# Kernel optimization log

Measured on AMD Instinct MI355X. Metric: run time of the kernel, lower is better.

## Reference

```python
import jax, jax.numpy as jnp
import numpy as np

B, T, I, U, O, BB = 256, 1024, 64, 256, 64, 128  # batch, seq, input, units, output, backbone_units

def lecun_tanh(x):
    return 1.7159 * jnp.tanh(0.666 * x)

def setup_inputs() -> dict:
    key = jax.random.key(0)
    ks = jax.random.split(key, 13)
    def lin(k, fan_in, fan_out):
        bound = 1.0 / np.sqrt(fan_in)
        kw, kb = jax.random.split(k)
        W = jax.random.uniform(kw, (fan_in, fan_out), jnp.float32, -bound, bound)
        b = jax.random.uniform(kb, (fan_out,), jnp.float32, -bound, bound)
        return W, b
    x = jax.random.normal(ks[0], (B, T, I), jnp.float32)
    W_bb, b_bb = lin(ks[1], I + U, BB)   # backbone Linear
    W_ff1, b_ff1 = lin(ks[2], BB, U)
    W_ff2, b_ff2 = lin(ks[3], BB, U)
    W_ta, b_ta = lin(ks[4], BB, U)       # time_a
    W_tb, b_tb = lin(ks[5], BB, U)       # time_b
    W_fc, b_fc = lin(ks[6], U, O)        # readout
    return {"x": x, "W_bb": W_bb, "b_bb": b_bb, "W_ff1": W_ff1, "b_ff1": b_ff1,
            "W_ff2": W_ff2, "b_ff2": b_ff2, "W_ta": W_ta, "b_ta": b_ta,
            "W_tb": W_tb, "b_tb": b_tb, "W_fc": W_fc, "b_fc": b_fc}

def reference(x, W_bb, b_bb, W_ff1, b_ff1, W_ff2, b_ff2, W_ta, b_ta, W_tb, b_tb, W_fc, b_fc):
    ts = jnp.float32(1.0)  # default elapsed time per step
    def step(h, xt):
        z = jnp.concatenate([xt, h], axis=-1)          # [B, I+U]
        g = lecun_tanh(z @ W_bb + b_bb)                # [B, BB]
        ff1 = jnp.tanh(g @ W_ff1 + b_ff1)              # [B, U]
        ff2 = jnp.tanh(g @ W_ff2 + b_ff2)
        t_interp = jax.nn.sigmoid((g @ W_ta + b_ta) * ts + (g @ W_tb + b_tb))
        h_new = ff1 * (1.0 - t_interp) + t_interp * ff2
        return h_new, h_new
    h0 = jnp.zeros((x.shape[0], U), x.dtype)
    h_last, hs = jax.lax.scan(step, h0, jnp.swapaxes(x, 0, 1))  # hs: [T, B, U]
    hs = jnp.swapaxes(hs, 0, 1)                                  # [B, T, U]
    out = hs @ W_fc + b_fc                                       # [B, T, O]
    return out, h_last
```

## Files before the change

kernel.cpp:

```cpp
#include <hip/hip_runtime.h>
#include <stdint.h>

#define B_ 256
#define T_ 1024
#define I_ 64
#define U_ 256
#define O_ 64
#define BB_ 128

typedef unsigned int u32;
typedef unsigned short u16;
typedef _Float16 half2_t __attribute__((ext_vector_type(2)));

#if defined(__has_builtin)
#if __has_builtin(__builtin_amdgcn_fdot2)
#define USE_DOT2 1
#else
#define USE_DOT2 0
#endif
#else
#define USE_DOT2 0
#endif

static __device__ __forceinline__ u32 packpair(float a, float b) {
  half2_t h; h.x = (_Float16)a; h.y = (_Float16)b;
  return __builtin_bit_cast(u32, h);
}
static __device__ __forceinline__ float unpack_lo(u32 u) {
  half2_t h = __builtin_bit_cast(half2_t, u); return (float)h.x;
}
static __device__ __forceinline__ float unpack_hi(u32 u) {
  half2_t h = __builtin_bit_cast(half2_t, u); return (float)h.y;
}
static __device__ __forceinline__ float dot2acc(u32 w, u32 z, float acc) {
#if USE_DOT2
  return __builtin_amdgcn_fdot2(__builtin_bit_cast(half2_t, w),
                                __builtin_bit_cast(half2_t, z), acc, false);
#else
  half2_t hw = __builtin_bit_cast(half2_t, w);
  half2_t hz = __builtin_bit_cast(half2_t, z);
  acc += (float)hw.x * (float)hz.x;
  acc += (float)hw.y * (float)hz.y;
  return acc;
#endif
}

template <int CTRL>
static __device__ __forceinline__ float dpp_mov_f(float v) {
  return __builtin_bit_cast(float, __builtin_amdgcn_update_dpp(
      0, __builtin_bit_cast(int, v), CTRL, 0xF, 0xF, true));
}
#define DPP_XOR1 0xB1
#define DPP_XOR2 0x4E
#define DPP_HMIR 0x141
#define DPP_MIRR 0x140

static __device__ __forceinline__ float fast_tanh(float x) {
  return 1.0f - 2.0f / (1.0f + __expf(2.0f * x));
}
static __device__ __forceinline__ float fast_sigmoid(float x) {
  return 1.0f / (1.0f + __expf(-x));
}

template <bool DEFER>
__global__ __launch_bounds__(1024)
void cfc_kernel(const float* __restrict__ x,
                const float* __restrict__ W_bb, const float* __restrict__ b_bb,
                const float* __restrict__ W_ff1, const float* __restrict__ b_ff1,
                const float* __restrict__ W_ff2, const float* __restrict__ b_ff2,
                const float* __restrict__ W_ta,  const float* __restrict__ b_ta,
                const float* __restrict__ W_tb,  const float* __restrict__ b_tb,
                const float* __restrict__ W_fc,  const float* __restrict__ b_fc,
                float* __restrict__ out, u32* __restrict__ Hbuf)
{
  __shared__ __align__(16) u32 s_z2[160];
  __shared__ __align__(16) u32 s_g2[64];
  u16* s_gh = (u16*)s_g2;

  const int tid = threadIdx.x;
  const int r   = blockIdx.x;

  const int ca  = tid >> 3;
  const int kga = tid & 7;
  const int jb = tid >> 2;
  const int kq = tid & 3;
  const int ro = tid >> 4;
  const int rk = tid & 15;

  u32 wbb[20];
#pragma unroll
  for (int j = 0; j < 5; ++j)
#pragma unroll
    for (int q = 0; q < 4; ++q) {
      int p = 4 * (kga + 8 * j) + q;
      wbb[4 * j + q] = packpair(W_bb[(2 * p) * BB_ + ca],
                                W_bb[(2 * p + 1) * BB_ + ca]);
    }
  u32 wf1[16], wf2[16], wta[16], wtb[16];
#pragma unroll
  for (int j = 0; j < 4; ++j)
#pragma unroll
    for (int q = 0; q < 4; ++q) {
      int p = 4 * (kq + 4 * j) + q;
      int k0 = 2 * p, k1 = 2 * p + 1;
      wf1[4 * j + q] = packpair(W_ff1[k0 * U_ + jb], W_ff1[k1 * U_ + jb]);
      wf2[4 * j + q] = packpair(W_ff2[k0 * U_ + jb], W_ff2[k1 * U_ + jb]);
      wta[4 * j + q] = packpair(W_ta [k0 * U_ + jb], W_ta [k1 * U_ + jb]);
      wtb[4 * j + q] = packpair(W_tb [k0 * U_ + jb], W_tb [k1 * U_ + jb]);
    }
  u32 wfc[8];
  float bfo = 0.f;
  if (!DEFER) {
#pragma unroll
    for (int j = 0; j < 2; ++j)
#pragma unroll
      for (int q = 0; q < 4; ++q) {
        int p = 4 * (rk + 16 * j) + q;
        wfc[4 * j + q] = packpair(W_fc[(2 * p) * O_ + ro],
                                  W_fc[(2 * p + 1) * O_ + ro]);
      }
    bfo = b_fc[ro];
  }
  const float bbbc = b_bb[ca];
  const float b1 = b_ff1[jb], b2 = b_ff2[jb];
  const float bta = b_ta[jb], btb = b_tb[jb];

  const float* xrow = x + (size_t)r * T_ * I_;
  const size_t out_row = (size_t)r * T_ * O_;
  u32* __restrict__ hrow = DEFER ? (Hbuf + (size_t)r * T_ * (U_ / 2)) : nullptr;

  if (tid < 160) s_z2[tid] = 0u;
  __syncthreads();
  if (tid < 32) {
    float2 xv = ((const float2*)xrow)[tid];
    s_z2[tid] = packpair(xv.x, xv.y);
  }
  __syncthreads();

  for (int t = 0; t < T_; ++t) {
    float2 xv;
    const bool ldx = (tid < 32) && (t + 1 < T_);
    if (ldx) xv = ((const float2*)(xrow + (size_t)(t + 1) * I_))[tid];

    float bacc = 0.f;
#pragma unroll
    for (int j = 0; j < 5; ++j) {
      uint4 zz = *reinterpret_cast<const uint4*>(s_z2 + 4 * (kga + 8 * j));
      bacc = dot2acc(wbb[4 * j + 0], zz.x, bacc);
      bacc = dot2acc(wbb[4 * j + 1], zz.y, bacc);
      bacc = dot2acc(wbb[4 * j + 2], zz.z, bacc);
      bacc = dot2acc(wbb[4 * j + 3], zz.w, bacc);
    }
    bacc += dpp_mov_f<DPP_XOR1>(bacc);
    bacc += dpp_mov_f<DPP_XOR2>(bacc);
    bacc += dpp_mov_f<DPP_HMIR>(bacc);
    float g = 1.7159f * fast_tanh(0.666f * (bacc + bbbc));

    float racc = 0.f;
    if (!DEFER) {
#pragma unroll
      for (int j = 0; j < 2; ++j) {
        uint4 hh = *reinterpret_cast<const uint4*>(s_z2 + 32 + 4 * (rk + 16 * j));
        racc = dot2acc(wfc[4 * j + 0], hh.x, racc);
        racc = dot2acc(wfc[4 * j + 1], hh.y, racc);
        racc = dot2acc(wfc[4 * j + 2], hh.z, racc);
        racc = dot2acc(wfc[4 * j + 3], hh.w, racc);
      }
      racc += dpp_mov_f<DPP_XOR1>(racc);
      racc += dpp_mov_f<DPP_XOR2>(racc);
      racc += dpp_mov_f<DPP_HMIR>(racc);
      racc += dpp_mov_f<DPP_MIRR>(racc);
    }
    if ((tid & 7) == 0)
      s_gh[ca] = __builtin_bit_cast(u16, (_Float16)g);
    if (!DEFER && t > 0 && rk == 0)
      out[out_row + (size_t)(t - 1) * O_ + ro] = racc + bfo;
    __syncthreads();

    float a1 = 0.f, a2 = 0.f, a3 = 0.f, a4 = 0.f;
#pragma unroll
    for (int j = 0; j < 4; ++j) {
      uint4 gg = *reinterpret_cast<const uint4*>(s_g2 + 4 * (kq + 4 * j));
      a1 = dot2acc(wf1[4 * j + 0], gg.x, a1);
      a1 = dot2acc(wf1[4 * j + 1], gg.y, a1);
      a1 = dot2acc(wf1[4 * j + 2], gg.z, a1);
      a1 = dot2acc(wf1[4 * j + 3], gg.w, a1);
      a2 = dot2acc(wf2[4 * j + 0], gg.x, a2);
      a2 = dot2acc(wf2[4 * j + 1], gg.y, a2);
      a2 = dot2acc(wf2[4 * j + 2], gg.z, a2);
      a2 = dot2acc(wf2[4 * j + 3], gg.w, a2);
      a3 = dot2acc(wta[4 * j + 0], gg.x, a3);
      a3 = dot2acc(wta[4 * j + 1], gg.y, a3);
      a3 = dot2acc(wta[4 * j + 2], gg.z, a3);
      a3 = dot2acc(wta[4 * j + 3], gg.w, a3);
      a4 = dot2acc(wtb[4 * j + 0], gg.x, a4);
      a4 = dot2acc(wtb[4 * j + 1], gg.y, a4);
      a4 = dot2acc(wtb[4 * j + 2], gg.z, a4);
      a4 = dot2acc(wtb[4 * j + 3], gg.w, a4);
    }
    a1 += dpp_mov_f<DPP_XOR1>(a1); a1 += dpp_mov_f<DPP_XOR2>(a1);
    a2 += dpp_mov_f<DPP_XOR1>(a2); a2 += dpp_mov_f<DPP_XOR2>(a2);
    a3 += dpp_mov_f<DPP_XOR1>(a3); a3 += dpp_mov_f<DPP_XOR2>(a3);
    a4 += dpp_mov_f<DPP_XOR1>(a4); a4 += dpp_mov_f<DPP_XOR2>(a4);
    float f1 = fast_tanh(a1 + b1);
    float f2 = fast_tanh(a2 + b2);
    float ti = fast_sigmoid(a3 + bta + a4 + btb);
    float h  = f1 + ti * (f2 - f1);
    float hq = dpp_mov_f<DPP_HMIR>(h);

    if ((tid & 7) == 0) {
      u32 pr = packpair(h, hq);
      int m = tid >> 3;
      s_z2[32 + m] = pr;
      if (DEFER) hrow[(size_t)t * (U_ / 2) + m] = pr;
    }
    if (ldx) s_z2[tid] = packpair(xv.x, xv.y);
    __syncthreads();
  }

  if (!DEFER) {
    float racc = 0.f;
#pragma unroll
    for (int j = 0; j < 2; ++j) {
      uint4 hh = *reinterpret_cast<const uint4*>(s_z2 + 32 + 4 * (rk + 16 * j));
      racc = dot2acc(wfc[4 * j + 0], hh.x, racc);
      racc = dot2acc(wfc[4 * j + 1], hh.y, racc);
      racc = dot2acc(wfc[4 * j + 2], hh.z, racc);
      racc = dot2acc(wfc[4 * j + 3], hh.w, racc);
    }
    racc += dpp_mov_f<DPP_XOR1>(racc);
    racc += dpp_mov_f<DPP_XOR2>(racc);
    racc += dpp_mov_f<DPP_HMIR>(racc);
    racc += dpp_mov_f<DPP_MIRR>(racc);
    if (rk == 0)
      out[out_row + (size_t)(T_ - 1) * O_ + ro] = racc + bfo;
  }

  if (tid < 128) {
    u32 hp = s_z2[32 + tid];
    float2 hv; hv.x = unpack_lo(hp); hv.y = unpack_hi(hp);
    ((float2*)(out + (size_t)B_ * T_ * O_))[r * 128 + tid] = hv;
  }
}

__global__ __launch_bounds__(512)
void ro_kernel(const u32* __restrict__ Hbuf,
               const float* __restrict__ W_fc, const float* __restrict__ b_fc,
               float* __restrict__ out)
{
  __shared__ __align__(16) u32 s_h[8 * 128];
  const int tid = threadIdx.x;
  const int o   = tid & 63;
  const int w   = tid >> 6;
  const int r   = blockIdx.x;

  u32 wfc[128];
#pragma unroll
  for (int p = 0; p < 128; ++p)
    wfc[p] = packpair(W_fc[(2 * p) * O_ + o], W_fc[(2 * p + 1) * O_ + o]);
  const float bo = b_fc[o];

  const u32* hrow = Hbuf + (size_t)r * T_ * 128;
  const size_t out_row = (size_t)r * T_ * O_;

  for (int c = 0; c < T_ / 8; ++c) {
    *(uint2*)(s_h + 2 * tid) =
        *(const uint2*)(hrow + (size_t)c * 1024 + 2 * tid);
    __syncthreads();
    float acc = bo;
    const uint4* h4 = reinterpret_cast<const uint4*>(s_h + w * 128);
#pragma unroll
    for (int i = 0; i < 32; ++i) {
      uint4 hh = h4[i];
      acc = dot2acc(wfc[4 * i + 0], hh.x, acc);
      acc = dot2acc(wfc[4 * i + 1], hh.y, acc);
      acc = dot2acc(wfc[4 * i + 2], hh.z, acc);
      acc = dot2acc(wfc[4 * i + 3], hh.w, acc);
    }
    out[out_row + (size_t)(8 * c + w) * O_ + o] = acc;
    __syncthreads();
  }
}

extern "C" void kernel_launch(void* const* d_in, const int* in_sizes, int n_in,
                              void* d_out, int out_size, void* d_ws, size_t ws_size,
                              hipStream_t stream) {
  const float* x     = (const float*)d_in[0];
  const float* W_bb  = (const float*)d_in[1];
  const float* b_bb  = (const float*)d_in[2];
  const float* W_ff1 = (const float*)d_in[3];
  const float* b_ff1 = (const float*)d_in[4];
  const float* W_ff2 = (const float*)d_in[5];
  const float* b_ff2 = (const float*)d_in[6];
  const float* W_ta  = (const float*)d_in[7];
  const float* b_ta  = (const float*)d_in[8];
  const float* W_tb  = (const float*)d_in[9];
  const float* b_tb  = (const float*)d_in[10];
  const float* W_fc  = (const float*)d_in[11];
  const float* b_fc  = (const float*)d_in[12];
  float* out = (float*)d_out;

  const size_t h_bytes = (size_t)B_ * T_ * (U_ / 2) * sizeof(u32);
  if (ws_size >= h_bytes) {
    u32* Hbuf = (u32*)d_ws;
    cfc_kernel<true><<<dim3(B_), dim3(1024), 0, stream>>>(
        x, W_bb, b_bb, W_ff1, b_ff1, W_ff2, b_ff2,
        W_ta, b_ta, W_tb, b_tb, W_fc, b_fc, out, Hbuf);
    ro_kernel<<<dim3(B_), dim3(512), 0, stream>>>(Hbuf, W_fc, b_fc, out);
  } else {
    cfc_kernel<false><<<dim3(B_), dim3(1024), 0, stream>>>(
        x, W_bb, b_bb, W_ff1, b_ff1, W_ff2, b_ff2,
        W_ta, b_ta, W_tb, b_tb, W_fc, b_fc, out, nullptr);
  }
}
```

Measured before the change: 1.901 ms.

## Replace per-row recurrent kernel with MFMA kernel processing 16 batch rows per block

Adds a new recurrence kernel in which each 512-thread block handles 16 batch rows and computes the backbone and the three head matmuls with 16x16x32 f16 MFMA instructions. Weights stay in registers as packed f16, and the ta and tb weights are pre-summed so one matmul serves both. The activations use exp2 and reciprocal intrinsics with scale factors folded into the constants. The change trades the previous one-row-per-block scalar and dot2 path, launched as 256 blocks, for matrix cores over only 16 blocks, so it runs on far fewer compute units.

```diff
diff --git a/kernel.cpp b/kernel.cpp
--- a/kernel.cpp
+++ b/kernel.cpp
@@ -11,6 +11,8 @@
 typedef unsigned int u32;
 typedef unsigned short u16;
 typedef _Float16 half2_t __attribute__((ext_vector_type(2)));
+typedef _Float16 f16x8 __attribute__((ext_vector_type(8)));
+typedef float f32x4 __attribute__((ext_vector_type(4)));
 
 #if defined(__has_builtin)
 #if __has_builtin(__builtin_amdgcn_fdot2)
@@ -60,6 +62,210 @@
 }
 static __device__ __forceinline__ float fast_sigmoid(float x) {
   return 1.0f / (1.0f + __expf(-x));
+}
+
+static __device__ __forceinline__ float rcpf(float x) {
+#if defined(__has_builtin) && __has_builtin(__builtin_amdgcn_rcpf)
+  return __builtin_amdgcn_rcpf(x);
+#else
+  return 1.0f / x;
+#endif
+}
+static __device__ __forceinline__ float exp2fast(float x) {
+#if defined(__has_builtin) && __has_builtin(__builtin_amdgcn_exp2f)
+  return __builtin_amdgcn_exp2f(x);
+#else
+  return exp2f(x);
+#endif
+}
+
+static __device__ __forceinline__ f32x4 mfma16(uint4 a, uint4 b, f32x4 c) {
+  return __builtin_amdgcn_mfma_f32_16x16x32_f16(
+      __builtin_bit_cast(f16x8, a), __builtin_bit_cast(f16x8, b), c, 0, 0, 0);
+}
+
+#define LOG2E 1.44269504f
+
+__global__ __launch_bounds__(512, 2)
+void cfc_mfma(const float* __restrict__ x,
+              const float* __restrict__ W_bb, const float* __restrict__ b_bb,
+              const float* __restrict__ W_ff1, const float* __restrict__ b_ff1,
+              const float* __restrict__ W_ff2, const float* __restrict__ b_ff2,
+              const float* __restrict__ W_ta,  const float* __restrict__ b_ta,
+              const float* __restrict__ W_tb,  const float* __restrict__ b_tb,
+              float* __restrict__ out, u32* __restrict__ Hbuf)
+{
+  __shared__ __align__(16) u32 s_z[2560];
+  __shared__ __align__(16) u32 s_g[1024];
+
+  const int tid = threadIdx.x;
+  const int l   = tid & 63;
+  const int w   = tid >> 6;
+  const int c16 = l & 15;
+  const int q4  = l >> 4;
+  const int odd = l & 1;
+  const int row0 = blockIdx.x * 16;
+
+  uint4 wbb[10];
+  {
+    const int colb = w * 16 + c16;
+#pragma unroll
+    for (int c = 0; c < 10; ++c) {
+      u32 qv[4];
+#pragma unroll
+      for (int q = 0; q < 4; ++q) {
+        const int k0 = c * 32 + q4 * 8 + 2 * q;
+        qv[q] = packpair(W_bb[(size_t)k0 * BB_ + colb],
+                         W_bb[(size_t)(k0 + 1) * BB_ + colb]);
+      }
+      wbb[c] = make_uint4(qv[0], qv[1], qv[2], qv[3]);
+    }
+  }
+  uint4 wff[3][2][4];
+#pragma unroll
+  for (int ut = 0; ut < 2; ++ut) {
+    const int u = w * 32 + ut * 16 + c16;
+#pragma unroll
+    for (int c = 0; c < 4; ++c) {
+      u32 qa[4], qb[4], qc[4];
+#pragma unroll
+      for (int q = 0; q < 4; ++q) {
+        const int k0 = c * 32 + q4 * 8 + 2 * q;
+        const size_t i0 = (size_t)k0 * U_ + u, i1 = i0 + U_;
+        qa[q] = packpair(W_ff1[i0], W_ff1[i1]);
+        qb[q] = packpair(W_ff2[i0], W_ff2[i1]);
+        qc[q] = packpair(W_ta[i0] + W_tb[i0], W_ta[i1] + W_tb[i1]);
+      }
+      wff[0][ut][c] = make_uint4(qa[0], qa[1], qa[2], qa[3]);
+      wff[1][ut][c] = make_uint4(qb[0], qb[1], qb[2], qb[3]);
+      wff[2][ut][c] = make_uint4(qc[0], qc[1], qc[2], qc[3]);
+    }
+  }
+
+  const float bgs = b_bb[w * 16 + c16] * (1.332f * LOG2E);
+  float b1s[2], b2s[2], btn[2];
+#pragma unroll
+  for (int ut = 0; ut < 2; ++ut) {
+    const int u = w * 32 + ut * 16 + c16;
+    b1s[ut] = b_ff1[u] * (2.0f * LOG2E);
+    b2s[ut] = b_ff2[u] * (2.0f * LOG2E);
+    btn[ut] = -(b_ta[u] + b_tb[u]) * LOG2E;
+  }
+
+  const int mx = tid >> 5, px = tid & 31;
+  const float* xptr = x + (size_t)(row0 + mx) * T_ * I_ + 2 * px;
+  const int zxw = ((px >> 4) * 64 + mx + 16 * ((px >> 2) & 3)) * 4 + (px & 3);
+
+  const int rbase = odd ? 2 : 0;
+  const int m0 = q4 * 4 + rbase, m1 = m0 + 1;
+  const int pg = w * 8 + (c16 >> 1);
+  const int gw0 = ((pg >> 4) * 64 + 16 * ((pg >> 2) & 3)) * 4 + (pg & 3)
+                  + 16 * q4 + (odd ? 8 : 0);
+  int zw_[2]; size_t hb0_[2], hb1_[2];
+#pragma unroll
+  for (int ut = 0; ut < 2; ++ut) {
+    const int pu = w * 16 + ut * 8 + (c16 >> 1);
+    zw_[ut] = ((2 + (pu >> 4)) * 64 + 16 * ((pu >> 2) & 3)) * 4 + (pu & 3)
+              + 16 * q4 + (odd ? 8 : 0);
+    hb0_[ut] = (size_t)(row0 + m0) * T_ * 128 + pu;
+    hb1_[ut] = (size_t)(row0 + m1) * T_ * 128 + pu;
+  }
+
+  reinterpret_cast<uint4*>(s_z)[128 + tid] = make_uint4(0u, 0u, 0u, 0u);
+  {
+    float2 xv = *(const float2*)xptr;
+    s_z[zxw] = packpair(xv.x, xv.y);
+  }
+  __syncthreads();
+
+  const uint4* z4 = (const uint4*)s_z;
+  const uint4* g4 = (const uint4*)s_g;
+
+  for (int t = 0; t < T_; ++t) {
+    float2 xv;
+    const bool ldx = (t + 1 < T_);
+    if (ldx) xv = *(const float2*)(xptr + (size_t)(t + 1) * I_);
+
+    f32x4 aA = {0.f, 0.f, 0.f, 0.f}, aB = {0.f, 0.f, 0.f, 0.f};
+#pragma unroll
+    for (int c = 0; c < 10; c += 2) {
+      aA = mfma16(z4[c * 64 + l],       wbb[c],     aA);
+      aB = mfma16(z4[(c + 1) * 64 + l], wbb[c + 1], aB);
+    }
+    const f32x4 ab = aA + aB;
+
+    u32 gq[4];
+#pragma unroll
+    for (int r = 0; r < 4; ++r) {
+      const float a  = __builtin_fmaf(ab[r], 1.332f * LOG2E, bgs);
+      const float rr = rcpf(exp2fast(a) + 1.0f);
+      const float g  = __builtin_fmaf(rr, -3.4318f, 1.7159f);
+      const float gp = dpp_mov_f<DPP_XOR1>(g);
+      gq[r] = odd ? packpair(gp, g) : packpair(g, gp);
+    }
+    s_g[gw0]     = odd ? gq[2] : gq[0];
+    s_g[gw0 + 4] = odd ? gq[3] : gq[1];
+    __syncthreads();
+
+    f32x4 af[3][2];
+#pragma unroll
+    for (int mt = 0; mt < 3; ++mt)
+#pragma unroll
+      for (int ut = 0; ut < 2; ++ut)
+        af[mt][ut] = (f32x4){0.f, 0.f, 0.f, 0.f};
+#pragma unroll
+    for (int c = 0; c < 4; ++c) {
+      const uint4 ga = g4[c * 64 + l];
+#pragma unroll
+      for (int mt = 0; mt < 3; ++mt)
+#pragma unroll
+        for (int ut = 0; ut < 2; ++ut)
+          af[mt][ut] = mfma16(ga, wff[mt][ut][c], af[mt][ut]);
+    }
+
+#pragma unroll
+    for (int ut = 0; ut < 2; ++ut) {
+      u32 hq[4];
+#pragma unroll
+      for (int r = 0; r < 4; ++r) {
+        const float a1 = __builtin_fmaf(af[0][ut][r], 2.0f * LOG2E, b1s[ut]);
+        const float f1 = __builtin_fmaf(rcpf(exp2fast(a1) + 1.0f), -2.0f, 1.0f);
+        const float a2 = __builtin_fmaf(af[1][ut][r], 2.0f * LOG2E, b2s[ut]);
+        const float f2 = __builtin_fmaf(rcpf(exp2fast(a2) + 1.0f), -2.0f, 1.0f);
+        const float at = __builtin_fmaf(af[2][ut][r], -LOG2E, btn[ut]);
+        const float ti = rcpf(exp2fast(at) + 1.0f);
+        const float h  = __builtin_fmaf(ti, f2 - f1, f1);
+        const float hp = dpp_mov_f<DPP_XOR1>(h);
+        hq[r] = odd ? packpair(hp, h) : packpair(h, hp);
+      }
+      const u32 s0 = odd ? hq[2] : hq[0];
+      const u32 s1 = odd ? hq[3] : hq[1];
+      s_z[zw_[ut]]     = s0;
+      s_z[zw_[ut] + 4] = s1;
+      Hbuf[hb0_[ut] + (size_t)t * 128] = s0;
+      Hbuf[hb1_[ut] + (size_t)t * 128] = s1;
+    }
+    if (ldx) s_z[zxw] = packpair(xv.x, xv.y);
+    __syncthreads();
+  }
+
+  {
+    const uint4 hv = reinterpret_cast<const uint4*>(s_z)[128 + tid];
+    float2* tail = (float2*)(out + (size_t)B_ * T_ * O_);
+#pragma unroll
+    for (int i = 0; i < 4; ++i) {
+      const int vh   = tid * 4 + i;
+      const int ch   = vh >> 8;
+      const int lane = (vh >> 2) & 63;
+      const int slot = vh & 3;
+      const int m    = lane & 15;
+      const int bq   = lane >> 4;
+      const int pu   = ch * 16 + bq * 4 + slot;
+      const u32 hp   = (i == 0) ? hv.x : (i == 1) ? hv.y : (i == 2) ? hv.z : hv.w;
+      float2 hf; hf.x = unpack_lo(hp); hf.y = unpack_hi(hp);
+      tail[(size_t)(row0 + m) * 128 + pu] = hf;
+    }
+  }
 }
 
 template <bool DEFER>
@@ -303,9 +509,9 @@
   const size_t h_bytes = (size_t)B_ * T_ * (U_ / 2) * sizeof(u32);
   if (ws_size >= h_bytes) {
     u32* Hbuf = (u32*)d_ws;
-    cfc_kernel<true><<<dim3(B_), dim3(1024), 0, stream>>>(
+    cfc_mfma<<<dim3(B_ / 16), dim3(512), 0, stream>>>(
         x, W_bb, b_bb, W_ff1, b_ff1, W_ff2, b_ff2,
-        W_ta, b_ta, W_tb, b_tb, W_fc, b_fc, out, Hbuf);
+        W_ta, b_ta, W_tb, b_tb, out, Hbuf);
     ro_kernel<<<dim3(B_), dim3(512), 0, stream>>>(Hbuf, W_fc, b_fc, out);
   } else {
     cfc_kernel<false><<<dim3(B_), dim3(1024), 0, stream>>>(
```

Measured after the change: 1.831 ms. 1.04x faster.
